# Performance work log

Hardware: AMD Instinct MI355X
Metric: run time of the kernel (lower is better)

The kernel has to match this reference:

```python
import jax, jax.numpy as jnp
import numpy as np

K = 8192   # out_features
N = 8192   # in_features
GS = 64    # group_size (quantization groups along N)
NG = N // GS
M = 64     # tokens (small -> dequant-traffic dominated)
QMAX = 16  # 2**nbits for nbits=4


def setup_inputs() -> dict:
    key = jax.random.key(0)
    ks = jax.random.split(key, 8)
    x = jax.random.normal(ks[0], (M, N), dtype=jnp.float32)
    W_q = jax.random.randint(ks[1], (K, N), 0, QMAX, dtype=jnp.int32).astype(jnp.int8)
    scales = jax.random.uniform(ks[2], (K, NG, 1), dtype=jnp.float32, minval=0.01, maxval=0.1)
    zeros = jax.random.uniform(ks[3], (K, NG, 1), dtype=jnp.float32, minval=0.0, maxval=15.0)
    mask = jax.random.bernoulli(ks[4], 0.65, (K, N)).astype(jnp.float32)
    mu1 = jax.random.uniform(ks[5], (N,), dtype=jnp.float32, minval=0.5, maxval=2.0)
    mu2 = jax.random.uniform(ks[6], (K,), dtype=jnp.float32, minval=0.5, maxval=2.0)
    bias = jax.random.normal(ks[7], (K,), dtype=jnp.float32)
    return {"x": x, "W_q": W_q, "scales": scales, "zeros": zeros,
            "mask": mask, "mu1": mu1, "mu2": mu2, "bias": bias}


def reference(x, W_q, scales, zeros, mask, mu1, mu2, bias):
    Kd, Nd = W_q.shape
    ng = scales.shape[1]
    gs = Nd // ng
    # group-wise dequant: (q - zero) * scale, groups along input dim
    Qg = W_q.astype(jnp.float32).reshape(Kd, ng, gs)            # [K, NG, GS]
    W_deq = ((Qg - zeros) * scales).reshape(Kd, Nd)             # [K, N]
    # sinkhorn rescale + sparsity mask
    W_deq = W_deq * mu2[:, None] * mu1[None, :] * mask          # [K, N]
    W_deq = W_deq.astype(x.dtype)
    # nn.functional.linear: y = x @ W^T + b
    return x @ W_deq.T + bias
```

## Files before the change

kernel.cpp:

```cpp
#include <hip/hip_runtime.h>
#include <stdint.h>

typedef __attribute__((ext_vector_type(8))) short short8;
typedef __attribute__((ext_vector_type(4))) float f32x4;
typedef __attribute__((ext_vector_type(2))) unsigned int u32x2;
typedef __attribute__((ext_vector_type(4))) unsigned int u32x4;

#define KDIM 8192
#define NDIM 8192
#define MDIM 64
#define NGRP 128
#define KT 64
#define SPLIT 8
#define NCHUNK (NDIM / SPLIT)
#define NSTEPS (NCHUNK / 64)
#define XFRAG (MDIM * NDIM)
#define MK (MDIM * KDIM)

__device__ __forceinline__ short f2bf(float v) {
  unsigned u = __builtin_bit_cast(unsigned, v);
  u += 0x7FFFu + ((u >> 16) & 1u);
  return (short)(u >> 16);
}
__device__ __forceinline__ float bf2f(short h) {
  unsigned u = ((unsigned)(unsigned short)h) << 16;
  return __builtin_bit_cast(float, u);
}

__global__ void init_out_kernel(const float* __restrict__ bias, float* __restrict__ out) {
  int i = blockIdx.x * blockDim.x + threadIdx.x;
  f32x4 b = ((const f32x4*)bias)[i & (KDIM / 4 - 1)];
  ((f32x4*)out)[i] = b;
}

__global__ void reduce_kernel(const float* __restrict__ pw, const float* __restrict__ bias,
                              float* __restrict__ out) {
  int i = blockIdx.x * blockDim.x + threadIdx.x;
  f32x4 acc = ((const f32x4*)bias)[i & (KDIM / 4 - 1)];
#pragma unroll
  for (int s = 0; s < SPLIT; ++s) acc += ((const f32x4*)pw)[s * (MK / 4) + i];
  ((f32x4*)out)[i] = acc;
}

__global__ void prep_xf_kernel(const float* __restrict__ x, const float* __restrict__ mu1,
                               short* __restrict__ xfH, short* __restrict__ xfL) {
  int tid = blockIdx.x * blockDim.x + threadIdx.x;
  int l = tid & 63;
  int mblk = (tid >> 6) & 3;
  int nblk = tid >> 8;
  int m = mblk * 16 + (l & 15);
  int nb = nblk * 32 + (l >> 4) * 8;
  const float* xr = x + (size_t)m * NDIM + nb;
  f32x4 x0 = *(const f32x4*)xr;
  f32x4 x1 = *(const f32x4*)(xr + 4);
  f32x4 u0 = *(const f32x4*)(mu1 + nb);
  f32x4 u1 = *(const f32x4*)(mu1 + nb + 4);
  short8 hv, lv;
#pragma unroll
  for (int i = 0; i < 8; ++i) {
    float xv = (i < 4) ? x0[i & 3] * u0[i & 3] : x1[i & 3] * u1[i & 3];
    short h = f2bf(xv);
    hv[i] = h;
    lv[i] = f2bf(xv - bf2f(h));
  }
  *(short8*)(xfH + (size_t)tid * 8) = hv;
  *(short8*)(xfL + (size_t)tid * 8) = lv;
}


struct StepRegs {
  f32x4 m[4];
  u32x2 q8[2];
  float sz, zz;
};

__device__ __forceinline__ void load_step(int st, const float* __restrict__ mrow,
                                          const uint8_t* __restrict__ q8row,
                                          const float* __restrict__ srow,
                                          const float* __restrict__ zrow, StepRegs& r) {
  const int off = st * 64;
#pragma unroll
  for (int sub = 0; sub < 2; ++sub) {
    r.m[sub * 2] = *(const f32x4*)(mrow + off + sub * 32);
    r.m[sub * 2 + 1] = *(const f32x4*)(mrow + off + sub * 32 + 4);
    r.q8[sub] = *(const u32x2*)(q8row + off + sub * 32);
  }
  r.sz = srow[st];
  r.zz = zrow[st];
}

template <bool ATOMIC>
__device__ __forceinline__ void compute_step(const StepRegs& r, float mu2k, int nblk0,
                                             const short8* __restrict__ a8H,
                                             const short8* __restrict__ a8L, int l,
                                             f32x4 acc[4]) {
  const float se = r.sz * mu2k;
  const float nz = -r.zz * se;
#pragma unroll
  for (int sub = 0; sub < 2; ++sub) {
    const short8* apH = a8H + (size_t)(nblk0 + sub) * 256 + l;
    const short8* apL = a8L + (size_t)(nblk0 + sub) * 256 + l;
    short8 ah0 = apH[0], ah1 = apH[64], ah2 = apH[128], ah3 = apH[192];
    short8 al0 = apL[0], al1 = apL[64], al2 = apL[128], al3 = apL[192];
    const unsigned qw0 = r.q8[sub][0], qw1 = r.q8[sub][1];
    short8 bh, bl;
#pragma unroll
    for (int i = 0; i < 8; ++i) {
      float qf = (float)((((i < 4) ? qw0 : qw1) >> (8 * (i & 3))) & 0xFFu);
      float mv = r.m[sub * 2 + (i >> 2)][i & 3];
      float wv = fmaf(qf, se, nz) * mv;
      short h = f2bf(wv);
      bh[i] = h;
      bl[i] = f2bf(wv - bf2f(h));
    }
    acc[0] = __builtin_amdgcn_mfma_f32_16x16x32_bf16(ah0, bh, acc[0], 0, 0, 0);
    acc[0] = __builtin_amdgcn_mfma_f32_16x16x32_bf16(ah0, bl, acc[0], 0, 0, 0);
    acc[0] = __builtin_amdgcn_mfma_f32_16x16x32_bf16(al0, bh, acc[0], 0, 0, 0);
    acc[1] = __builtin_amdgcn_mfma_f32_16x16x32_bf16(ah1, bh, acc[1], 0, 0, 0);
    acc[1] = __builtin_amdgcn_mfma_f32_16x16x32_bf16(ah1, bl, acc[1], 0, 0, 0);
    acc[1] = __builtin_amdgcn_mfma_f32_16x16x32_bf16(al1, bh, acc[1], 0, 0, 0);
    acc[2] = __builtin_amdgcn_mfma_f32_16x16x32_bf16(ah2, bh, acc[2], 0, 0, 0);
    acc[2] = __builtin_amdgcn_mfma_f32_16x16x32_bf16(ah2, bl, acc[2], 0, 0, 0);
    acc[2] = __builtin_amdgcn_mfma_f32_16x16x32_bf16(al2, bh, acc[2], 0, 0, 0);
    acc[3] = __builtin_amdgcn_mfma_f32_16x16x32_bf16(ah3, bh, acc[3], 0, 0, 0);
    acc[3] = __builtin_amdgcn_mfma_f32_16x16x32_bf16(ah3, bl, acc[3], 0, 0, 0);
    acc[3] = __builtin_amdgcn_mfma_f32_16x16x32_bf16(al3, bh, acc[3], 0, 0, 0);
  }
}

template <bool ATOMIC>
__device__ __forceinline__ void gemm_body_i8(const uint8_t* __restrict__ wq,
                                             const float* __restrict__ scales,
                                             const float* __restrict__ zeros,
                                             const float* __restrict__ mask,
                                             const float* __restrict__ mu2,
                                             const short* __restrict__ xfH,
                                             const short* __restrict__ xfL,
                                             float* __restrict__ outp) {
  const int bx = blockIdx.x;
  const int kt = bx >> 3;
  const int s = bx & 7;
  const int k0 = kt * KT;
  const int n0 = s * NCHUNK;
  const int tid = threadIdx.x;
  const int w = tid >> 6;
  const int l = tid & 63;
  const int row = l & 15;
  const int g4 = l >> 4;
  const int kc = k0 + w * 16 + row;
  const float mu2k = mu2[kc];

  const float* mrow = mask + (size_t)kc * NDIM + n0 + g4 * 8;
  const uint8_t* q8row = wq + (size_t)kc * NDIM + n0 + g4 * 8;
  const float* srow = scales + (size_t)kc * NGRP + (n0 >> 6);
  const float* zrow = zeros + (size_t)kc * NGRP + (n0 >> 6);
  const short8* a8H = (const short8*)xfH;
  const short8* a8L = (const short8*)xfL;

  f32x4 acc[4] = {};
  StepRegs A, B;

  load_step(0, mrow, q8row, srow, zrow, A);
  const int nb0 = n0 >> 5;
#pragma unroll 1
  for (int st = 0; st < NSTEPS; st += 2) {
    load_step(st + 1, mrow, q8row, srow, zrow, B);
    compute_step<ATOMIC>(A, mu2k, nb0 + st * 2, a8H, a8L, l, acc);
    if (st + 2 < NSTEPS) load_step(st + 2, mrow, q8row, srow, zrow, A);
    compute_step<ATOMIC>(B, mu2k, nb0 + st * 2 + 2, a8H, a8L, l, acc);
  }

#pragma unroll
  for (int mb = 0; mb < 4; ++mb) {
#pragma unroll
    for (int j = 0; j < 4; ++j) {
      int m = mb * 16 + g4 * 4 + j;
      if constexpr (ATOMIC)
        atomicAdd(outp + (size_t)m * KDIM + kc, acc[mb][j]);
      else
        outp[(size_t)s * MK + (size_t)m * KDIM + kc] = acc[mb][j];
    }
  }
}

template <bool ATOMIC>
__device__ void gemm_body_i32(const int* __restrict__ wq, const float* __restrict__ scales,
                              const float* __restrict__ zeros, const float* __restrict__ mask,
                              const float* __restrict__ mu2, const short* __restrict__ xfH,
                              const short* __restrict__ xfL, float* __restrict__ outp) {
  const int bx = blockIdx.x;
  const int kt = bx >> 3, s = bx & 7;
  const int k0 = kt * KT, n0 = s * NCHUNK;
  const int tid = threadIdx.x;
  const int w = tid >> 6, l = tid & 63;
  const int row = l & 15, g4 = l >> 4;
  const int kc = k0 + w * 16 + row;
  const float mu2k = mu2[kc];
  const float* mrow = mask + (size_t)kc * NDIM + n0 + g4 * 8;
  const int* qrow = wq + (size_t)kc * NDIM + n0 + g4 * 8;
  const float* srow = scales + (size_t)kc * NGRP + (n0 >> 6);
  const float* zrow = zeros + (size_t)kc * NGRP + (n0 >> 6);
  const short8* a8H = (const short8*)xfH;
  const short8* a8L = (const short8*)xfL;
  f32x4 acc[4] = {};
  for (int st = 0; st < NSTEPS; ++st) {
    const int off = st * 64;
    const float se = srow[st] * mu2k, nz = -zrow[st] * se;
#pragma unroll
    for (int sub = 0; sub < 2; ++sub) {
      f32x4 m0 = *(const f32x4*)(mrow + off + sub * 32);
      f32x4 m1 = *(const f32x4*)(mrow + off + sub * 32 + 4);
      u32x4 qa = *(const u32x4*)(qrow + off + sub * 32);
      u32x4 qb = *(const u32x4*)(qrow + off + sub * 32 + 4);
      short8 bh, bl;
#pragma unroll
      for (int i = 0; i < 8; ++i) {
        float qf = (float)(int)((i < 4) ? qa[i & 3] : qb[i & 3]);
        float mv = (i < 4) ? m0[i & 3] : m1[i & 3];
        float wv = fmaf(qf, se, nz) * mv;
        short h = f2bf(wv);
        bh[i] = h;
        bl[i] = f2bf(wv - bf2f(h));
      }
      const int nblk0 = (n0 + off) >> 5;
      const short8* apH = a8H + (size_t)(nblk0 + sub) * 256 + l;
      const short8* apL = a8L + (size_t)(nblk0 + sub) * 256 + l;
#pragma unroll
      for (int mb = 0; mb < 4; ++mb) {
        short8 ah = apH[mb * 64], al = apL[mb * 64];
        acc[mb] = __builtin_amdgcn_mfma_f32_16x16x32_bf16(ah, bh, acc[mb], 0, 0, 0);
        acc[mb] = __builtin_amdgcn_mfma_f32_16x16x32_bf16(ah, bl, acc[mb], 0, 0, 0);
        acc[mb] = __builtin_amdgcn_mfma_f32_16x16x32_bf16(al, bh, acc[mb], 0, 0, 0);
      }
    }
  }
#pragma unroll
  for (int mb = 0; mb < 4; ++mb) {
#pragma unroll
    for (int j = 0; j < 4; ++j) {
      int m = mb * 16 + g4 * 4 + j;
      if constexpr (ATOMIC)
        atomicAdd(outp + (size_t)m * KDIM + kc, acc[mb][j]);
      else
        outp[(size_t)s * MK + (size_t)m * KDIM + kc] = acc[mb][j];
    }
  }
}

template <bool ATOMIC>
__global__ void __launch_bounds__(256, 4) gemm_kernel(
    const void* __restrict__ wq, const float* __restrict__ scales,
    const float* __restrict__ zeros, const float* __restrict__ mask,
    const float* __restrict__ mu2, const short* __restrict__ xfH,
    const short* __restrict__ xfL, float* __restrict__ outp) {
  const unsigned* wqu = (const unsigned*)wq;
  bool i32m = true;
#pragma unroll
  for (int i = 0; i < 16; ++i) i32m &= (wqu[i] <= 15u);
  if (i32m)
    gemm_body_i32<ATOMIC>((const int*)wq, scales, zeros, mask, mu2, xfH, xfL, outp);
  else
    gemm_body_i8<ATOMIC>((const uint8_t*)wq, scales, zeros, mask, mu2, xfH, xfL, outp);
}

extern "C" void kernel_launch(void* const* d_in, const int* in_sizes, int n_in,
                              void* d_out, int out_size, void* d_ws, size_t ws_size,
                              hipStream_t stream) {
  const float* x = (const float*)d_in[0];
  const void* wq = d_in[1];
  const float* scales = (const float*)d_in[2];
  const float* zeros = (const float*)d_in[3];
  const float* mask = (const float*)d_in[4];
  const float* mu1 = (const float*)d_in[5];
  const float* mu2 = (const float*)d_in[6];
  const float* bias = (const float*)d_in[7];
  float* out = (float*)d_out;
  short* xfH = (short*)d_ws;
  short* xfL = xfH + XFRAG;
  float* pw = (float*)(xfL + XFRAG);

  const size_t need_ws = 2u * XFRAG * sizeof(short) + (size_t)SPLIT * MK * sizeof(float);
  const bool use_ws = ws_size >= need_ws;

  prep_xf_kernel<<<dim3(256), dim3(256), 0, stream>>>(x, mu1, xfH, xfL);
  if (use_ws) {
    gemm_kernel<false><<<dim3((KDIM / KT) * SPLIT), dim3(256), 0, stream>>>(
        wq, scales, zeros, mask, mu2, xfH, xfL, pw);
    reduce_kernel<<<dim3(512), dim3(256), 0, stream>>>(pw, bias, out);
  } else {
    init_out_kernel<<<dim3(512), dim3(256), 0, stream>>>(bias, out);
    gemm_kernel<true><<<dim3((KDIM / KT) * SPLIT), dim3(256), 0, stream>>>(
        wq, scales, zeros, mask, mu2, xfH, xfL, out);
  }
}
```

Before: 572.4 us.

## Stage mask, weights and activations through LDS with async global_load_lds double buffering

The int8 GEMM path now stages mask, quantized weights, scales/zeros and the split-bf16 activation fragments into shared memory using direct global-to-LDS loads, double-buffered two steps ahead with explicit vmcnt waits and barriers. The activation prep layout and the per-lane column mapping are changed so each lane reads contiguous 16-element chunks, giving wider coalesced transfers. The aim is to hide global memory latency behind the MFMA work. In exchange it uses 64KB of LDS per block, lowers the launch bound to 2 blocks per CU, and adds two barriers per step.

```diff
diff --git a/kernel.cpp b/kernel.cpp
--- a/kernel.cpp
+++ b/kernel.cpp
@@ -3,7 +3,6 @@
 
 typedef __attribute__((ext_vector_type(8))) short short8;
 typedef __attribute__((ext_vector_type(4))) float f32x4;
-typedef __attribute__((ext_vector_type(2))) unsigned int u32x2;
 typedef __attribute__((ext_vector_type(4))) unsigned int u32x4;
 
 #define KDIM 8192
@@ -17,6 +16,15 @@
 #define XFRAG (MDIM * NDIM)
 #define MK (MDIM * KDIM)
 
+#define MB_OFF 0
+#define WQ_OFF 32768
+#define XF_OFF 40960
+#define SC_OFF 57344
+#define LDS_BYTES 65536
+
+#define AS3 __attribute__((address_space(3)))
+#define AS1 __attribute__((address_space(1)))
+
 __device__ __forceinline__ short f2bf(float v) {
   unsigned u = __builtin_bit_cast(unsigned, v);
   u += 0x7FFFu + ((u >> 16) & 1u);
@@ -47,9 +55,10 @@
   int tid = blockIdx.x * blockDim.x + threadIdx.x;
   int l = tid & 63;
   int mblk = (tid >> 6) & 3;
-  int nblk = tid >> 8;
+  int g = tid >> 9;
+  int sub = (tid >> 8) & 1;
   int m = mblk * 16 + (l & 15);
-  int nb = nblk * 32 + (l >> 4) * 8;
+  int nb = g * 64 + (l >> 4) * 16 + sub * 8;
   const float* xr = x + (size_t)m * NDIM + nb;
   f32x4 x0 = *(const f32x4*)xr;
   f32x4 x1 = *(const f32x4*)(xr + 4);
@@ -67,66 +76,6 @@
   *(short8*)(xfL + (size_t)tid * 8) = lv;
 }
 
-
-struct StepRegs {
-  f32x4 m[4];
-  u32x2 q8[2];
-  float sz, zz;
-};
-
-__device__ __forceinline__ void load_step(int st, const float* __restrict__ mrow,
-                                          const uint8_t* __restrict__ q8row,
-                                          const float* __restrict__ srow,
-                                          const float* __restrict__ zrow, StepRegs& r) {
-  const int off = st * 64;
-#pragma unroll
-  for (int sub = 0; sub < 2; ++sub) {
-    r.m[sub * 2] = *(const f32x4*)(mrow + off + sub * 32);
-    r.m[sub * 2 + 1] = *(const f32x4*)(mrow + off + sub * 32 + 4);
-    r.q8[sub] = *(const u32x2*)(q8row + off + sub * 32);
-  }
-  r.sz = srow[st];
-  r.zz = zrow[st];
-}
-
-template <bool ATOMIC>
-__device__ __forceinline__ void compute_step(const StepRegs& r, float mu2k, int nblk0,
-                                             const short8* __restrict__ a8H,
-                                             const short8* __restrict__ a8L, int l,
-                                             f32x4 acc[4]) {
-  const float se = r.sz * mu2k;
-  const float nz = -r.zz * se;
-#pragma unroll
-  for (int sub = 0; sub < 2; ++sub) {
-    const short8* apH = a8H + (size_t)(nblk0 + sub) * 256 + l;
-    const short8* apL = a8L + (size_t)(nblk0 + sub) * 256 + l;
-    short8 ah0 = apH[0], ah1 = apH[64], ah2 = apH[128], ah3 = apH[192];
-    short8 al0 = apL[0], al1 = apL[64], al2 = apL[128], al3 = apL[192];
-    const unsigned qw0 = r.q8[sub][0], qw1 = r.q8[sub][1];
-    short8 bh, bl;
-#pragma unroll
-    for (int i = 0; i < 8; ++i) {
-      float qf = (float)((((i < 4) ? qw0 : qw1) >> (8 * (i & 3))) & 0xFFu);
-      float mv = r.m[sub * 2 + (i >> 2)][i & 3];
-      float wv = fmaf(qf, se, nz) * mv;
-      short h = f2bf(wv);
-      bh[i] = h;
-      bl[i] = f2bf(wv - bf2f(h));
-    }
-    acc[0] = __builtin_amdgcn_mfma_f32_16x16x32_bf16(ah0, bh, acc[0], 0, 0, 0);
-    acc[0] = __builtin_amdgcn_mfma_f32_16x16x32_bf16(ah0, bl, acc[0], 0, 0, 0);
-    acc[0] = __builtin_amdgcn_mfma_f32_16x16x32_bf16(al0, bh, acc[0], 0, 0, 0);
-    acc[1] = __builtin_amdgcn_mfma_f32_16x16x32_bf16(ah1, bh, acc[1], 0, 0, 0);
-    acc[1] = __builtin_amdgcn_mfma_f32_16x16x32_bf16(ah1, bl, acc[1], 0, 0, 0);
-    acc[1] = __builtin_amdgcn_mfma_f32_16x16x32_bf16(al1, bh, acc[1], 0, 0, 0);
-    acc[2] = __builtin_amdgcn_mfma_f32_16x16x32_bf16(ah2, bh, acc[2], 0, 0, 0);
-    acc[2] = __builtin_amdgcn_mfma_f32_16x16x32_bf16(ah2, bl, acc[2], 0, 0, 0);
-    acc[2] = __builtin_amdgcn_mfma_f32_16x16x32_bf16(al2, bh, acc[2], 0, 0, 0);
-    acc[3] = __builtin_amdgcn_mfma_f32_16x16x32_bf16(ah3, bh, acc[3], 0, 0, 0);
-    acc[3] = __builtin_amdgcn_mfma_f32_16x16x32_bf16(ah3, bl, acc[3], 0, 0, 0);
-    acc[3] = __builtin_amdgcn_mfma_f32_16x16x32_bf16(al3, bh, acc[3], 0, 0, 0);
-  }
-}
 
 template <bool ATOMIC>
 __device__ __forceinline__ void gemm_body_i8(const uint8_t* __restrict__ wq,
@@ -136,7 +85,7 @@
                                              const float* __restrict__ mu2,
                                              const short* __restrict__ xfH,
                                              const short* __restrict__ xfL,
-                                             float* __restrict__ outp) {
+                                             float* __restrict__ outp, char* smem) {
   const int bx = blockIdx.x;
   const int kt = bx >> 3;
   const int s = bx & 7;
@@ -145,29 +94,111 @@
   const int tid = threadIdx.x;
   const int w = tid >> 6;
   const int l = tid & 63;
-  const int row = l & 15;
+  const int r = l & 15;
   const int g4 = l >> 4;
-  const int kc = k0 + w * 16 + row;
+  const int kc = k0 + w * 16 + r;
   const float mu2k = mu2[kc];
 
-  const float* mrow = mask + (size_t)kc * NDIM + n0 + g4 * 8;
-  const uint8_t* q8row = wq + (size_t)kc * NDIM + n0 + g4 * 8;
-  const float* srow = scales + (size_t)kc * NGRP + (n0 >> 6);
-  const float* zrow = zeros + (size_t)kc * NGRP + (n0 >> 6);
-  const short8* a8H = (const short8*)xfH;
-  const short8* a8L = (const short8*)xfL;
+  AS3 char* lb = (AS3 char*)smem;
+
+  const float* msrc = mask + (size_t)kc * NDIM + n0 + (l >> 4) * 4;
+  const uint8_t* qsrc = wq + (size_t)kc * NDIM + n0 + (l >> 4) * 16;
+  const float* ssrc = scales + (size_t)(k0 + w * 16 + (l >> 2)) * NGRP + (n0 >> 6) + (l & 3) * 4;
+  const float* zsrc = zeros + (size_t)(k0 + w * 16 + (l >> 2)) * NGRP + (n0 >> 6) + (l & 3) * 4;
+  const int nb0 = s * 32;
+
+#define GLDS16(gp, loff) \
+  __builtin_amdgcn_global_load_lds((const AS1 void*)(gp), (AS3 void*)(lb + (loff)), 16, 0, 0)
+
+#define STAGE_MW(st_, buf_)                                                            \
+  do {                                                                                 \
+    const float* mp_ = msrc + (st_) * 64;                                              \
+    _Pragma("unroll") for (int q_ = 0; q_ < 4; ++q_)                                   \
+        GLDS16(mp_ + q_ * 16, MB_OFF + (buf_) * 16384 + w * 4096 + q_ * 1024);         \
+    GLDS16(qsrc + (st_) * 64, WQ_OFF + (buf_) * 4096 + w * 1024);                      \
+  } while (0)
+
+#define STAGE_XF(st_)                                                                  \
+  do {                                                                                 \
+    _Pragma("unroll") for (int ii_ = 0; ii_ < 4; ++ii_) {                              \
+      int t_ = 2 * w + (ii_ >> 1);                                                     \
+      int hl_ = ii_ & 1;                                                               \
+      int F_ = (nb0 + (st_) * 2 + (t_ >> 2));                                          \
+      const short* sp_ = (hl_ ? xfL : xfH) + ((size_t)F_ * 256 + (t_ & 3) * 64 + l) * 8; \
+      GLDS16(sp_, XF_OFF + t_ * 2048 + hl_ * 1024);                                    \
+    }                                                                                  \
+  } while (0)
+
+  GLDS16(ssrc, SC_OFF + w * 2048);
+  GLDS16(zsrc, SC_OFF + w * 2048 + 1024);
+  STAGE_XF(0);
+  STAGE_MW(0, 0);
+  STAGE_MW(1, 1);
 
   f32x4 acc[4] = {};
-  StepRegs A, B;
-
-  load_step(0, mrow, q8row, srow, zrow, A);
-  const int nb0 = n0 >> 5;
-#pragma unroll 1
-  for (int st = 0; st < NSTEPS; st += 2) {
-    load_step(st + 1, mrow, q8row, srow, zrow, B);
-    compute_step<ATOMIC>(A, mu2k, nb0 + st * 2, a8H, a8L, l, acc);
-    if (st + 2 < NSTEPS) load_step(st + 2, mrow, q8row, srow, zrow, A);
-    compute_step<ATOMIC>(B, mu2k, nb0 + st * 2 + 2, a8H, a8L, l, acc);
+
+#define LDF4(off) (*(const f32x4*)(smem + (off)))
+#define LDS8(off) (*(const short8*)(smem + (off)))
+#define LDU4(off) (*(const u32x4*)(smem + (off)))
+#define LDF(off) (*(const float*)(smem + (off)))
+
+#pragma unroll 2
+  for (int st = 0; st < NSTEPS; ++st) {
+    const int cur = st & 1;
+    if (st + 1 < NSTEPS) {
+      asm volatile("s_waitcnt vmcnt(5)" ::: "memory");
+    } else {
+      asm volatile("s_waitcnt vmcnt(0)" ::: "memory");
+    }
+    __builtin_amdgcn_s_barrier();
+    asm volatile("" ::: "memory");
+
+    const unsigned mbase = (unsigned)(MB_OFF + cur * 16384 + w * 4096 + g4 * 1024 + r * 16);
+    f32x4 mq[4];
+#pragma unroll
+    for (int sub = 0; sub < 2; ++sub)
+#pragma unroll
+      for (int jj = 0; jj < 2; ++jj) mq[sub * 2 + jj] = LDF4(mbase + sub * 512 + jj * 256);
+    u32x4 wqv = LDU4(WQ_OFF + cur * 4096 + w * 1024 + l * 16);
+    short8 xh[2][4], xl[2][4];
+#pragma unroll
+    for (int t = 0; t < 8; ++t) {
+      xh[t >> 2][t & 3] = LDS8(XF_OFF + t * 2048 + l * 16);
+      xl[t >> 2][t & 3] = LDS8(XF_OFF + t * 2048 + 1024 + l * 16);
+    }
+    const unsigned soff = (unsigned)(SC_OFF + w * 2048 + (4 * r + (st >> 2)) * 16 + (st & 3) * 4);
+    float sc = LDF(soff);
+    float zc = LDF(soff + 1024);
+
+    asm volatile("s_waitcnt lgkmcnt(0)" ::: "memory");
+    __builtin_amdgcn_s_barrier();
+    asm volatile("" ::: "memory");
+
+    if (st + 1 < NSTEPS) STAGE_XF(st + 1);
+    if (st + 2 < NSTEPS) STAGE_MW(st + 2, cur);
+
+    const float se = sc * mu2k;
+    const float nz = -zc * se;
+#pragma unroll
+    for (int sub = 0; sub < 2; ++sub) {
+      short8 bh, bl;
+#pragma unroll
+      for (int b = 0; b < 8; ++b) {
+        unsigned wbits = (b < 4) ? wqv[sub * 2] : wqv[sub * 2 + 1];
+        float qf = (float)((wbits >> (8 * (b & 3))) & 0xFFu);
+        float mv = mq[sub * 2 + (b >> 2)][b & 3];
+        float wv = fmaf(qf, se, nz) * mv;
+        short h = f2bf(wv);
+        bh[b] = h;
+        bl[b] = f2bf(wv - bf2f(h));
+      }
+#pragma unroll
+      for (int mb = 0; mb < 4; ++mb) {
+        acc[mb] = __builtin_amdgcn_mfma_f32_16x16x32_bf16(xh[sub][mb], bh, acc[mb], 0, 0, 0);
+        acc[mb] = __builtin_amdgcn_mfma_f32_16x16x32_bf16(xh[sub][mb], bl, acc[mb], 0, 0, 0);
+        acc[mb] = __builtin_amdgcn_mfma_f32_16x16x32_bf16(xl[sub][mb], bh, acc[mb], 0, 0, 0);
+      }
+    }
   }
 
 #pragma unroll
@@ -181,6 +212,13 @@
         outp[(size_t)s * MK + (size_t)m * KDIM + kc] = acc[mb][j];
     }
   }
+#undef GLDS16
+#undef STAGE_MW
+#undef STAGE_XF
+#undef LDF4
+#undef LDS8
+#undef LDU4
+#undef LDF
 }
 
 template <bool ATOMIC>
@@ -193,25 +231,25 @@
   const int k0 = kt * KT, n0 = s * NCHUNK;
   const int tid = threadIdx.x;
   const int w = tid >> 6, l = tid & 63;
-  const int row = l & 15, g4 = l >> 4;
-  const int kc = k0 + w * 16 + row;
+  const int r = l & 15, g4 = l >> 4;
+  const int kc = k0 + w * 16 + r;
   const float mu2k = mu2[kc];
-  const float* mrow = mask + (size_t)kc * NDIM + n0 + g4 * 8;
-  const int* qrow = wq + (size_t)kc * NDIM + n0 + g4 * 8;
+  const float* mrow = mask + (size_t)kc * NDIM + n0 + g4 * 16;
+  const int* qrow = wq + (size_t)kc * NDIM + n0 + g4 * 16;
   const float* srow = scales + (size_t)kc * NGRP + (n0 >> 6);
   const float* zrow = zeros + (size_t)kc * NGRP + (n0 >> 6);
   const short8* a8H = (const short8*)xfH;
   const short8* a8L = (const short8*)xfL;
   f32x4 acc[4] = {};
   for (int st = 0; st < NSTEPS; ++st) {
-    const int off = st * 64;
     const float se = srow[st] * mu2k, nz = -zrow[st] * se;
 #pragma unroll
     for (int sub = 0; sub < 2; ++sub) {
-      f32x4 m0 = *(const f32x4*)(mrow + off + sub * 32);
-      f32x4 m1 = *(const f32x4*)(mrow + off + sub * 32 + 4);
-      u32x4 qa = *(const u32x4*)(qrow + off + sub * 32);
-      u32x4 qb = *(const u32x4*)(qrow + off + sub * 32 + 4);
+      const int fo = st * 64 + sub * 8;
+      f32x4 m0 = *(const f32x4*)(mrow + fo);
+      f32x4 m1 = *(const f32x4*)(mrow + fo + 4);
+      u32x4 qa = *(const u32x4*)(qrow + fo);
+      u32x4 qb = *(const u32x4*)(qrow + fo + 4);
       short8 bh, bl;
 #pragma unroll
       for (int i = 0; i < 8; ++i) {
@@ -222,9 +260,9 @@
         bh[i] = h;
         bl[i] = f2bf(wv - bf2f(h));
       }
-      const int nblk0 = (n0 + off) >> 5;
-      const short8* apH = a8H + (size_t)(nblk0 + sub) * 256 + l;
-      const short8* apL = a8L + (size_t)(nblk0 + sub) * 256 + l;
+      const int F = s * 32 + st * 2 + sub;
+      const short8* apH = a8H + (size_t)F * 256 + l;
+      const short8* apL = a8L + (size_t)F * 256 + l;
 #pragma unroll
       for (int mb = 0; mb < 4; ++mb) {
         short8 ah = apH[mb * 64], al = apL[mb * 64];
@@ -248,11 +286,12 @@
 }
 
 template <bool ATOMIC>
-__global__ void __launch_bounds__(256, 4) gemm_kernel(
+__global__ void __launch_bounds__(256, 2) gemm_kernel(
     const void* __restrict__ wq, const float* __restrict__ scales,
     const float* __restrict__ zeros, const float* __restrict__ mask,
     const float* __restrict__ mu2, const short* __restrict__ xfH,
     const short* __restrict__ xfL, float* __restrict__ outp) {
+  __shared__ char smem[LDS_BYTES];
   const unsigned* wqu = (const unsigned*)wq;
   bool i32m = true;
 #pragma unroll
@@ -260,7 +299,7 @@
   if (i32m)
     gemm_body_i32<ATOMIC>((const int*)wq, scales, zeros, mask, mu2, xfH, xfL, outp);
   else
-    gemm_body_i8<ATOMIC>((const uint8_t*)wq, scales, zeros, mask, mu2, xfH, xfL, outp);
+    gemm_body_i8<ATOMIC>((const uint8_t*)wq, scales, zeros, mask, mu2, xfH, xfL, outp, smem);
 }
 
 extern "C" void kernel_launch(void* const* d_in, const int* in_sizes, int n_in,
```

Measured after the change: 593.3 us. +3.7%, slower.
